# Kernel optimization log

Hardware: AMD Instinct MI355X
Metric: run time of the kernel (lower is better)

Reference implementation:

```python
import jax, jax.numpy as jnp
import numpy as np

NUM_HEADS = 8
NEG_INF = -1e30


def _within_bucket_rank(idx):
    # idx: [U] int32 bucket ids; returns occurrence count of each id among earlier positions
    U = idx.shape[0]
    order = jnp.argsort(idx, stable=True)
    sv = idx[order]
    pos = jnp.arange(U, dtype=jnp.int32)
    is_start = jnp.concatenate([jnp.ones((1,), bool), sv[1:] != sv[:-1]])
    start = jax.lax.cummax(jnp.where(is_start, pos, 0))
    rank = pos - start
    return jnp.zeros(U, jnp.int32).at[order].set(rank)


def setup_inputs() -> dict:
    key = jax.random.key(0)
    ks = jax.random.split(key, 10)
    B, U, G, E = 8, 16384, 64, 128
    lin = jnp.linspace(0.0, 1.0, G)
    gx, gy = jnp.meshgrid(lin, lin, indexing='ij')
    xc_on_grid = jnp.broadcast_to(jnp.stack([gx, gy], -1), (B, G, G, 2)).astype(jnp.float32)
    s = 0.02
    return {
        'xc_off_grid': jax.random.uniform(ks[0], (B, U, 2), jnp.float32),
        'xc_on_grid': xc_on_grid,
        'zc_off_grid': jax.random.normal(ks[1], (B, U, E), jnp.float32),
        'zc_on_grid': jax.random.normal(ks[2], (B, G, G, E), jnp.float32),
        'latents': jax.random.normal(ks[3], (G * G, E), jnp.float32),
        'fake_embedding': jax.random.normal(ks[4], (E,), jnp.float32),
        'Wq': jax.random.normal(ks[5], (E, E), jnp.float32) * s,
        'Wk': jax.random.normal(ks[6], (E, E), jnp.float32) * s,
        'Wv': jax.random.normal(ks[7], (E, E), jnp.float32) * s,
        'Wo': jax.random.normal(ks[8], (E, E), jnp.float32) * s,
        'ignore_on_grid': 0,
    }


def _bucketize(xc_off_grid, xc_on_grid):
    # returns nearest flat grid index per off-grid point, shape [B, U] int32
    B = xc_off_grid.shape[0]
    dims = xc_on_grid.shape[1:-1]
    S = int(np.prod(dims))
    grid_shape = jnp.asarray(dims, jnp.float32)
    x_on = xc_on_grid.reshape(B, S, -1)
    xmin = x_on.min(axis=(0, 1))
    xmax = x_on.max(axis=(0, 1))
    spacing = (xmax - xmin) / (grid_shape - 1.0)
    nm = jnp.floor((xc_off_grid - xmin + spacing / 2) / spacing)
    nm = jnp.clip(nm, 0.0, grid_shape - 1.0)
    # strides as in the original: flip(cumprod([1, *dims])[:-1])
    strides = np.flip(np.cumprod(np.concatenate([[1], np.asarray(dims)]))[:-1]).astype(np.float32)
    return (nm * jnp.asarray(strides)).sum(-1).astype(jnp.int32)


def _mhca(latents_q, kv, valid, Wq, Wk, Wv, Wo):
    # latents_q: [N,1,E], kv: [N,P,E], valid: [N,P] bool
    N, P, E = kv.shape
    H, Dh = NUM_HEADS, E // NUM_HEADS
    q = (latents_q @ Wq).reshape(N, 1, H, Dh)
    k = (kv @ Wk).reshape(N, P, H, Dh)
    v = (kv @ Wv).reshape(N, P, H, Dh)
    scores = jnp.einsum('nqhd,nkhd->nhqk', q, k) / jnp.sqrt(jnp.asarray(Dh, q.dtype))
    scores = jnp.where(valid[:, None, None, :], scores, NEG_INF)
    attn = jax.nn.softmax(scores, axis=-1)
    out = jnp.einsum('nhqk,nkhd->nqhd', attn, v).reshape(N, 1, E)
    return out @ Wo


def reference(xc_off_grid, xc_on_grid, zc_off_grid, zc_on_grid, latents, fake_embedding, Wq, Wk, Wv, Wo, ignore_on_grid):
    B, U, E = zc_off_grid.shape
    dims = xc_on_grid.shape[1:-1]
    S = int(np.prod(dims))
    z_on = zc_on_grid.reshape(B, S, E)

    nearest_idx = _bucketize(xc_off_grid, xc_on_grid)          # [B, U]
    cumcount = jax.vmap(_within_bucket_rank)(nearest_idx)       # [B, U]
    flat_seg = (nearest_idx + jnp.arange(B, dtype=jnp.int32)[:, None] * S).reshape(-1)
    counts = jax.ops.segment_sum(jnp.ones(B * U, jnp.int32), flat_seg, num_segments=B * S)
    max_patch = int(jax.device_get(counts.max())) + 1           # +1 slot for on-grid/fake token

    # ragged scatter of off-grid tokens into padded per-bucket buffer
    grid_stacked = jnp.zeros((B * S, max_patch, E), zc_off_grid.dtype)
    grid_stacked = grid_stacked.at[flat_seg, cumcount.reshape(-1)].set(zc_off_grid.reshape(B * U, E))
    if ignore_on_grid:
        last = jnp.broadcast_to(fake_embedding, (B * S, E))
    else:
        last = z_on.reshape(B * S, E)
    grid_stacked = grid_stacked.at[:, -1].set(last)

    slot = jnp.arange(max_patch)
    valid = (slot[None, :] < counts[:, None]) | (slot[None, :] == max_patch - 1)  # [B*S, P]

    lat = jnp.broadcast_to(latents[None], (B, S, E)).reshape(B * S, 1, E)
    zc = _mhca(lat, grid_stacked, valid, Wq, Wk, Wv, Wo)        # [B*S, 1, E]
    return zc.reshape(B, *dims, E)
```

## Files before the change

kernel.cpp:

```cpp
#include <hip/hip_runtime.h>
#include <math.h>

namespace {
constexpr int B_  = 8;
constexpr int U_  = 16384;
constexpr int S_  = 4096;
constexpr int E_  = 128;
constexpr int H_  = 8;
}

typedef __attribute__((ext_vector_type(8))) short bf16x8;
typedef __attribute__((ext_vector_type(4))) float f32x4;

__device__ inline unsigned short bf16rne(float x) {
  unsigned u = __float_as_uint(x);
  u = u + 0x7fffu + ((u >> 16) & 1u);
  return (unsigned short)(u >> 16);
}

__device__ inline bf16x8 pack8(float4 a, float4 b) {
  bf16x8 r;
  r[0] = (short)bf16rne(a.x); r[1] = (short)bf16rne(a.y);
  r[2] = (short)bf16rne(a.z); r[3] = (short)bf16rne(a.w);
  r[4] = (short)bf16rne(b.x); r[5] = (short)bf16rne(b.y);
  r[6] = (short)bf16rne(b.z); r[7] = (short)bf16rne(b.w);
  return r;
}

__global__ __launch_bounds__(256) void prep_weights(
    const float* __restrict__ Wq, const float* __restrict__ Wk,
    const float* __restrict__ Wv, const float* __restrict__ Wo,
    unsigned short* __restrict__ dst) {
  const int i = blockIdx.x * 256 + threadIdx.x;
  const int w = i >> 14, e = i & 16383;
  const int k = e >> 7, n = e & 127;
  const float* src = (w == 0) ? Wq : (w == 1) ? Wk : (w == 2) ? Wv : Wo;
  dst[w * 16384 + (((k >> 3) * 128 + n) << 3) + (k & 7)] = bf16rne(src[e]);
}

__global__ __launch_bounds__(256, 4) void qproj_mfma(
    const float* __restrict__ latents, const unsigned short* __restrict__ Wq_sw,
    float* __restrict__ Q) {
  __shared__ __align__(16) unsigned short wq[16384];
  const int tid = threadIdx.x;
  {
    const uint4* s = (const uint4*)Wq_sw;
    uint4* d = (uint4*)wq;
#pragma unroll
    for (int i = 0; i < 8; ++i) d[i * 256 + tid] = s[i * 256 + tid];
  }
  __syncthreads();

  const int wave = tid >> 6, lane = tid & 63;
  const int c = lane & 15, g = lane >> 4;
  const int t0w = blockIdx.x * 64 + wave * 16;

  f32x4 acc[8];
#pragma unroll
  for (int i = 0; i < 8; ++i) acc[i] = {0.f, 0.f, 0.f, 0.f};

  const float* arow = latents + (size_t)(t0w + c) * E_ + g * 8;
  const bf16x8* bq = (const bf16x8*)wq;
#pragma unroll
  for (int ks = 0; ks < 4; ++ks) {
    float4 a0 = *(const float4*)(arow + ks * 32);
    float4 a1 = *(const float4*)(arow + ks * 32 + 4);
    bf16x8 af = pack8(a0, a1);
    const int bo = (ks * 4 + g) * 128 + c;
#pragma unroll
    for (int nt = 0; nt < 8; ++nt)
      acc[nt] = __builtin_amdgcn_mfma_f32_16x16x32_bf16(af, bq[bo + nt * 16], acc[nt], 0, 0, 0);
  }
#pragma unroll
  for (int nt = 0; nt < 8; ++nt)
#pragma unroll
    for (int r = 0; r < 4; ++r)
      Q[(size_t)(t0w + g * 4 + r) * E_ + nt * 16 + c] = acc[nt][r] * 0.25f;
}

__global__ __launch_bounds__(256, 2) void ongrid_mfma(
    const float* __restrict__ zc_on, const float* __restrict__ fake,
    const int* __restrict__ ignore_flag,
    const unsigned short* __restrict__ Wk_sw, const unsigned short* __restrict__ Wv_sw,
    const float* __restrict__ Q,
    float* __restrict__ num, float* __restrict__ denom) {
  __shared__ __align__(16) unsigned short wk[16384];
  __shared__ __align__(16) unsigned short wv[16384];
  const int tid = threadIdx.x;
  {
    const uint4* sk = (const uint4*)Wk_sw;
    const uint4* sv = (const uint4*)Wv_sw;
    uint4* dk = (uint4*)wk; uint4* dv = (uint4*)wv;
#pragma unroll
    for (int i = 0; i < 8; ++i) {
      dk[i * 256 + tid] = sk[i * 256 + tid];
      dv[i * 256 + tid] = sv[i * 256 + tid];
    }
  }
  const int ign = *ignore_flag;
  __syncthreads();

  const int wave = tid >> 6, lane = tid & 63;
  const int c = lane & 15, g = lane >> 4;
  const int t0w = blockIdx.x * 64 + wave * 16;

  f32x4 accK[8], accV[8];
#pragma unroll
  for (int i = 0; i < 8; ++i) { accK[i] = {0.f,0.f,0.f,0.f}; accV[i] = {0.f,0.f,0.f,0.f}; }

  const float* arow = ign ? (fake + g * 8)
                          : (zc_on + (size_t)(t0w + c) * E_ + g * 8);
  const bf16x8* bk = (const bf16x8*)wk;
  const bf16x8* bv = (const bf16x8*)wv;
#pragma unroll
  for (int ks = 0; ks < 4; ++ks) {
    float4 a0 = *(const float4*)(arow + ks * 32);
    float4 a1 = *(const float4*)(arow + ks * 32 + 4);
    bf16x8 af = pack8(a0, a1);
    const int bo = (ks * 4 + g) * 128 + c;
#pragma unroll
    for (int nt = 0; nt < 8; ++nt) {
      accK[nt] = __builtin_amdgcn_mfma_f32_16x16x32_bf16(af, bk[bo + nt * 16], accK[nt], 0, 0, 0);
      accV[nt] = __builtin_amdgcn_mfma_f32_16x16x32_bf16(af, bv[bo + nt * 16], accV[nt], 0, 0, 0);
    }
  }

  float w_arr[8][4];
#pragma unroll
  for (int h = 0; h < 8; ++h)
#pragma unroll
    for (int r = 0; r < 4; ++r) {
      const int s = (t0w + g * 4 + r) & (S_ - 1);
      float p = accK[h][r] * Q[(size_t)s * E_ + h * 16 + c];
      p += __shfl_xor(p, 1, 64); p += __shfl_xor(p, 2, 64);
      p += __shfl_xor(p, 4, 64); p += __shfl_xor(p, 8, 64);
      w_arr[h][r] = __expf(p);
    }

#pragma unroll
  for (int nt = 0; nt < 8; ++nt)
#pragma unroll
    for (int r = 0; r < 4; ++r)
      num[(size_t)(t0w + g * 4 + r) * E_ + nt * 16 + c] = w_arr[nt][r] * accV[nt][r];

#pragma unroll
  for (int h = 0; h < 8; ++h)
    if (c == h) {
#pragma unroll
      for (int r = 0; r < 4; ++r)
        denom[(size_t)(t0w + g * 4 + r) * H_ + h] = w_arr[h][r];
    }
}

__global__ __launch_bounds__(256, 2) void offgrid_mfma(
    const float* __restrict__ xc_off, const float* __restrict__ zc_off,
    const unsigned short* __restrict__ Wk_sw, const unsigned short* __restrict__ Wv_sw,
    const float* __restrict__ Q,
    float* __restrict__ num, float* __restrict__ denom) {
  __shared__ __align__(16) unsigned short wk[16384];
  __shared__ __align__(16) unsigned short wv[16384];
  const int tid = threadIdx.x;
  {
    const uint4* sk = (const uint4*)Wk_sw;
    const uint4* sv = (const uint4*)Wv_sw;
    uint4* dk = (uint4*)wk; uint4* dv = (uint4*)wv;
#pragma unroll
    for (int i = 0; i < 8; ++i) {
      dk[i * 256 + tid] = sk[i * 256 + tid];
      dv[i * 256 + tid] = sv[i * 256 + tid];
    }
  }

  const int wave = tid >> 6, lane = tid & 63;
  const int c = lane & 15, g = lane >> 4;
  const int t0w = blockIdx.x * 64 + wave * 16;

  int seg_self;
  {
    const int tok = t0w + c;
    const int b = tok >> 14;
    const float sp = 1.0f / 63.0f;
    const float half = sp * 0.5f;
    const float x0 = xc_off[(size_t)tok * 2 + 0];
    const float x1 = xc_off[(size_t)tok * 2 + 1];
    float n0 = floorf((x0 - 0.0f + half) / sp);
    float n1 = floorf((x1 - 0.0f + half) / sp);
    n0 = fminf(fmaxf(n0, 0.0f), 63.0f);
    n1 = fminf(fmaxf(n1, 0.0f), 63.0f);
    seg_self = b * S_ + (int)(n0 * 64.0f + n1);
  }
  int seg[4];
#pragma unroll
  for (int r = 0; r < 4; ++r) seg[r] = __shfl(seg_self, g * 4 + r, 64);

  __syncthreads();

  f32x4 accK[8], accV[8];
#pragma unroll
  for (int i = 0; i < 8; ++i) { accK[i] = {0.f,0.f,0.f,0.f}; accV[i] = {0.f,0.f,0.f,0.f}; }

  const float* arow = zc_off + (size_t)(t0w + c) * E_ + g * 8;
  const bf16x8* bk = (const bf16x8*)wk;
  const bf16x8* bv = (const bf16x8*)wv;
#pragma unroll
  for (int ks = 0; ks < 4; ++ks) {
    float4 a0 = *(const float4*)(arow + ks * 32);
    float4 a1 = *(const float4*)(arow + ks * 32 + 4);
    bf16x8 af = pack8(a0, a1);
    const int bo = (ks * 4 + g) * 128 + c;
#pragma unroll
    for (int nt = 0; nt < 8; ++nt) {
      accK[nt] = __builtin_amdgcn_mfma_f32_16x16x32_bf16(af, bk[bo + nt * 16], accK[nt], 0, 0, 0);
      accV[nt] = __builtin_amdgcn_mfma_f32_16x16x32_bf16(af, bv[bo + nt * 16], accV[nt], 0, 0, 0);
    }
  }

  float w_arr[8][4];
#pragma unroll
  for (int h = 0; h < 8; ++h)
#pragma unroll
    for (int r = 0; r < 4; ++r) {
      const int s = seg[r] & (S_ - 1);
      float p = accK[h][r] * Q[(size_t)s * E_ + h * 16 + c];
      p += __shfl_xor(p, 1, 64); p += __shfl_xor(p, 2, 64);
      p += __shfl_xor(p, 4, 64); p += __shfl_xor(p, 8, 64);
      w_arr[h][r] = __expf(p);
    }

#pragma unroll
  for (int nt = 0; nt < 8; ++nt)
#pragma unroll
    for (int r = 0; r < 4; ++r)
      atomicAdd(&num[(size_t)seg[r] * E_ + nt * 16 + c], w_arr[nt][r] * accV[nt][r]);

#pragma unroll
  for (int h = 0; h < 8; ++h)
    if (c == h) {
#pragma unroll
      for (int r = 0; r < 4; ++r)
        atomicAdd(&denom[(size_t)seg[r] * H_ + h], w_arr[h][r]);
    }
}

__global__ __launch_bounds__(256, 4) void finalize_mfma(
    const unsigned short* __restrict__ Wo_sw, const float* __restrict__ denom,
    float* __restrict__ out) {
  __shared__ __align__(16) unsigned short wo[16384];
  const int tid = threadIdx.x;
  {
    const uint4* s = (const uint4*)Wo_sw;
    uint4* d = (uint4*)wo;
#pragma unroll
    for (int i = 0; i < 8; ++i) d[i * 256 + tid] = s[i * 256 + tid];
  }
  __syncthreads();

  const int wave = tid >> 6, lane = tid & 63;
  const int c = lane & 15, g = lane >> 4;
  const int t0w = blockIdx.x * 64 + wave * 16;

  f32x4 acc[8];
#pragma unroll
  for (int i = 0; i < 8; ++i) acc[i] = {0.f, 0.f, 0.f, 0.f};

  const float* nrow = out + (size_t)(t0w + c) * E_ + g * 8;
  const float* drow = denom + (size_t)(t0w + c) * H_;
  const bf16x8* bo_ = (const bf16x8*)wo;
#pragma unroll
  for (int ks = 0; ks < 4; ++ks) {
    const int head = (ks * 32 + g * 8) >> 4;
    const float dinv = 1.0f / drow[head];
    float4 a0 = *(const float4*)(nrow + ks * 32);
    float4 a1 = *(const float4*)(nrow + ks * 32 + 4);
    a0.x *= dinv; a0.y *= dinv; a0.z *= dinv; a0.w *= dinv;
    a1.x *= dinv; a1.y *= dinv; a1.z *= dinv; a1.w *= dinv;
    bf16x8 af = pack8(a0, a1);
    const int bofs = (ks * 4 + g) * 128 + c;
#pragma unroll
    for (int nt = 0; nt < 8; ++nt)
      acc[nt] = __builtin_amdgcn_mfma_f32_16x16x32_bf16(af, bo_[bofs + nt * 16], acc[nt], 0, 0, 0);
  }
#pragma unroll
  for (int nt = 0; nt < 8; ++nt)
#pragma unroll
    for (int r = 0; r < 4; ++r)
      out[(size_t)(t0w + g * 4 + r) * E_ + nt * 16 + c] = acc[nt][r];
}

extern "C" void kernel_launch(void* const* d_in, const int* in_sizes, int n_in,
                              void* d_out, int out_size, void* d_ws, size_t ws_size,
                              hipStream_t stream) {
  const float* xc_off  = (const float*)d_in[0];
  const float* zc_off  = (const float*)d_in[2];
  const float* zc_on   = (const float*)d_in[3];
  const float* latents = (const float*)d_in[4];
  const float* fake    = (const float*)d_in[5];
  const float* Wq      = (const float*)d_in[6];
  const float* Wk      = (const float*)d_in[7];
  const float* Wv      = (const float*)d_in[8];
  const float* Wo      = (const float*)d_in[9];
  const int*   ignore  = (const int*)d_in[10];

  float* out   = (float*)d_out;
  float* Q     = (float*)d_ws;
  float* denom = Q + (size_t)S_ * E_;
  unsigned short* Wsw = (unsigned short*)(denom + (size_t)B_ * S_ * H_);
  unsigned short* Wq_sw = Wsw;
  unsigned short* Wk_sw = Wsw + 16384;
  unsigned short* Wv_sw = Wsw + 32768;
  unsigned short* Wo_sw = Wsw + 49152;

  prep_weights<<<256, 256, 0, stream>>>(Wq, Wk, Wv, Wo, Wsw);
  qproj_mfma<<<S_ / 64, 256, 0, stream>>>(latents, Wq_sw, Q);
  ongrid_mfma<<<(B_ * S_) / 64, 256, 0, stream>>>(zc_on, fake, ignore, Wk_sw, Wv_sw, Q, out, denom);
  offgrid_mfma<<<(B_ * U_) / 64, 256, 0, stream>>>(xc_off, zc_off, Wk_sw, Wv_sw, Q, out, denom);
  finalize_mfma<<<(B_ * S_) / 64, 256, 0, stream>>>(Wo_sw, denom, out);
}
```

Baseline: 216.3 us.

## Permute Q layout for vectorized per-lane loads and double block size to 512

The Q projection output is stored permuted so each lane's eight per-head query values sit contiguously, letting the on-grid and off-grid kernels fetch them with two float4 loads up front instead of eight scattered scalar loads inside the score loop. All four MFMA kernels also move from 256 to 512 threads per block, handling 128 tokens per block. Each block's weight copy to LDS is then shared by twice as many tokens. Risks are higher register pressure from the preloaded Q values and lower occupancy from the new launch bounds.

Result: no change. 215.4 us (-0.4%).

```diff
diff --git a/kernel.cpp b/kernel.cpp
--- a/kernel.cpp
+++ b/kernel.cpp
@@ -38,22 +38,22 @@
   dst[w * 16384 + (((k >> 3) * 128 + n) << 3) + (k & 7)] = bf16rne(src[e]);
 }
 
-__global__ __launch_bounds__(256, 4) void qproj_mfma(
+__global__ __launch_bounds__(512, 4) void qproj_mfma(
     const float* __restrict__ latents, const unsigned short* __restrict__ Wq_sw,
-    float* __restrict__ Q) {
+    float* __restrict__ Qp) {
   __shared__ __align__(16) unsigned short wq[16384];
   const int tid = threadIdx.x;
   {
     const uint4* s = (const uint4*)Wq_sw;
     uint4* d = (uint4*)wq;
 #pragma unroll
-    for (int i = 0; i < 8; ++i) d[i * 256 + tid] = s[i * 256 + tid];
+    for (int i = 0; i < 4; ++i) d[i * 512 + tid] = s[i * 512 + tid];
   }
   __syncthreads();
 
   const int wave = tid >> 6, lane = tid & 63;
   const int c = lane & 15, g = lane >> 4;
-  const int t0w = blockIdx.x * 64 + wave * 16;
+  const int t0w = blockIdx.x * 128 + wave * 16;
 
   f32x4 acc[8];
 #pragma unroll
@@ -75,14 +75,14 @@
   for (int nt = 0; nt < 8; ++nt)
 #pragma unroll
     for (int r = 0; r < 4; ++r)
-      Q[(size_t)(t0w + g * 4 + r) * E_ + nt * 16 + c] = acc[nt][r] * 0.25f;
-}
-
-__global__ __launch_bounds__(256, 2) void ongrid_mfma(
+      Qp[(size_t)(t0w + g * 4 + r) * E_ + c * 8 + nt] = acc[nt][r] * 0.25f;
+}
+
+__global__ __launch_bounds__(512, 4) void ongrid_mfma(
     const float* __restrict__ zc_on, const float* __restrict__ fake,
     const int* __restrict__ ignore_flag,
     const unsigned short* __restrict__ Wk_sw, const unsigned short* __restrict__ Wv_sw,
-    const float* __restrict__ Q,
+    const float* __restrict__ Qp,
     float* __restrict__ num, float* __restrict__ denom) {
   __shared__ __align__(16) unsigned short wk[16384];
   __shared__ __align__(16) unsigned short wv[16384];
@@ -92,9 +92,9 @@
     const uint4* sv = (const uint4*)Wv_sw;
     uint4* dk = (uint4*)wk; uint4* dv = (uint4*)wv;
 #pragma unroll
-    for (int i = 0; i < 8; ++i) {
-      dk[i * 256 + tid] = sk[i * 256 + tid];
-      dv[i * 256 + tid] = sv[i * 256 + tid];
+    for (int i = 0; i < 4; ++i) {
+      dk[i * 512 + tid] = sk[i * 512 + tid];
+      dv[i * 512 + tid] = sv[i * 512 + tid];
     }
   }
   const int ign = *ignore_flag;
@@ -102,7 +102,15 @@
 
   const int wave = tid >> 6, lane = tid & 63;
   const int c = lane & 15, g = lane >> 4;
-  const int t0w = blockIdx.x * 64 + wave * 16;
+  const int t0w = blockIdx.x * 128 + wave * 16;
+
+  float4 qa[4], qb[4];
+#pragma unroll
+  for (int r = 0; r < 4; ++r) {
+    const int s = (t0w + g * 4 + r) & (S_ - 1);
+    qa[r] = *(const float4*)(Qp + (size_t)s * E_ + c * 8);
+    qb[r] = *(const float4*)(Qp + (size_t)s * E_ + c * 8 + 4);
+  }
 
   f32x4 accK[8], accV[8];
 #pragma unroll
@@ -130,8 +138,8 @@
   for (int h = 0; h < 8; ++h)
 #pragma unroll
     for (int r = 0; r < 4; ++r) {
-      const int s = (t0w + g * 4 + r) & (S_ - 1);
-      float p = accK[h][r] * Q[(size_t)s * E_ + h * 16 + c];
+      const float qv = (h < 4) ? qa[r][h] : qb[r][h - 4];
+      float p = accK[h][r] * qv;
       p += __shfl_xor(p, 1, 64); p += __shfl_xor(p, 2, 64);
       p += __shfl_xor(p, 4, 64); p += __shfl_xor(p, 8, 64);
       w_arr[h][r] = __expf(p);
@@ -152,10 +160,10 @@
     }
 }
 
-__global__ __launch_bounds__(256, 2) void offgrid_mfma(
+__global__ __launch_bounds__(512, 4) void offgrid_mfma(
     const float* __restrict__ xc_off, const float* __restrict__ zc_off,
     const unsigned short* __restrict__ Wk_sw, const unsigned short* __restrict__ Wv_sw,
-    const float* __restrict__ Q,
+    const float* __restrict__ Qp,
     float* __restrict__ num, float* __restrict__ denom) {
   __shared__ __align__(16) unsigned short wk[16384];
   __shared__ __align__(16) unsigned short wv[16384];
@@ -165,15 +173,15 @@
     const uint4* sv = (const uint4*)Wv_sw;
     uint4* dk = (uint4*)wk; uint4* dv = (uint4*)wv;
 #pragma unroll
-    for (int i = 0; i < 8; ++i) {
-      dk[i * 256 + tid] = sk[i * 256 + tid];
-      dv[i * 256 + tid] = sv[i * 256 + tid];
+    for (int i = 0; i < 4; ++i) {
+      dk[i * 512 + tid] = sk[i * 512 + tid];
+      dv[i * 512 + tid] = sv[i * 512 + tid];
     }
   }
 
   const int wave = tid >> 6, lane = tid & 63;
   const int c = lane & 15, g = lane >> 4;
-  const int t0w = blockIdx.x * 64 + wave * 16;
+  const int t0w = blockIdx.x * 128 + wave * 16;
 
   int seg_self;
   {
@@ -195,6 +203,14 @@
 
   __syncthreads();
 
+  float4 qa[4], qb[4];
+#pragma unroll
+  for (int r = 0; r < 4; ++r) {
+    const int s = seg[r] & (S_ - 1);
+    qa[r] = *(const float4*)(Qp + (size_t)s * E_ + c * 8);
+    qb[r] = *(const float4*)(Qp + (size_t)s * E_ + c * 8 + 4);
+  }
+
   f32x4 accK[8], accV[8];
 #pragma unroll
   for (int i = 0; i < 8; ++i) { accK[i] = {0.f,0.f,0.f,0.f}; accV[i] = {0.f,0.f,0.f,0.f}; }
@@ -220,8 +236,8 @@
   for (int h = 0; h < 8; ++h)
 #pragma unroll
     for (int r = 0; r < 4; ++r) {
-      const int s = seg[r] & (S_ - 1);
-      float p = accK[h][r] * Q[(size_t)s * E_ + h * 16 + c];
+      const float qv = (h < 4) ? qa[r][h] : qb[r][h - 4];
+      float p = accK[h][r] * qv;
       p += __shfl_xor(p, 1, 64); p += __shfl_xor(p, 2, 64);
       p += __shfl_xor(p, 4, 64); p += __shfl_xor(p, 8, 64);
       w_arr[h][r] = __expf(p);
@@ -242,7 +258,7 @@
     }
 }
 
-__global__ __launch_bounds__(256, 4) void finalize_mfma(
+__global__ __launch_bounds__(512, 4) void finalize_mfma(
     const unsigned short* __restrict__ Wo_sw, const float* __restrict__ denom,
     float* __restrict__ out) {
   __shared__ __align__(16) unsigned short wo[16384];
@@ -251,13 +267,13 @@
     const uint4* s = (const uint4*)Wo_sw;
     uint4* d = (uint4*)wo;
 #pragma unroll
-    for (int i = 0; i < 8; ++i) d[i * 256 + tid] = s[i * 256 + tid];
+    for (int i = 0; i < 4; ++i) d[i * 512 + tid] = s[i * 512 + tid];
   }
   __syncthreads();
 
   const int wave = tid >> 6, lane = tid & 63;
   const int c = lane & 15, g = lane >> 4;
-  const int t0w = blockIdx.x * 64 + wave * 16;
+  const int t0w = blockIdx.x * 128 + wave * 16;
 
   f32x4 acc[8];
 #pragma unroll
@@ -302,8 +318,8 @@
   const int*   ignore  = (const int*)d_in[10];
 
   float* out   = (float*)d_out;
-  float* Q     = (float*)d_ws;
-  float* denom = Q + (size_t)S_ * E_;
+  float* Qp    = (float*)d_ws;
+  float* denom = Qp + (size_t)S_ * E_;
   unsigned short* Wsw = (unsigned short*)(denom + (size_t)B_ * S_ * H_);
   unsigned short* Wq_sw = Wsw;
   unsigned short* Wk_sw = Wsw + 16384;
@@ -311,8 +327,8 @@
   unsigned short* Wo_sw = Wsw + 49152;
 
   prep_weights<<<256, 256, 0, stream>>>(Wq, Wk, Wv, Wo, Wsw);
-  qproj_mfma<<<S_ / 64, 256, 0, stream>>>(latents, Wq_sw, Q);
-  ongrid_mfma<<<(B_ * S_) / 64, 256, 0, stream>>>(zc_on, fake, ignore, Wk_sw, Wv_sw, Q, out, denom);
-  offgrid_mfma<<<(B_ * U_) / 64, 256, 0, stream>>>(xc_off, zc_off, Wk_sw, Wv_sw, Q, out, denom);
-  finalize_mfma<<<(B_ * S_) / 64, 256, 0, stream>>>(Wo_sw, denom, out);
-}
+  qproj_mfma<<<S_ / 128, 512, 0, stream>>>(latents, Wq_sw, Qp);
+  ongrid_mfma<<<(B_ * S_) / 128, 512, 0, stream>>>(zc_on, fake, ignore, Wk_sw, Wv_sw, Qp, out, denom);
+  offgrid_mfma<<<(B_ * U_) / 128, 512, 0, stream>>>(xc_off, zc_off, Wk_sw, Wv_sw, Qp, out, denom);
+  finalize_mfma<<<(B_ * S_) / 128, 512, 0, stream>>>(Wo_sw, denom, out);
+}
```
